# Kernel tuning notes

Hardware: AMD Instinct MI355X
Metric: run time of the kernel (lower is better)

Reference implementation:

```python
import jax, jax.numpy as jnp
import numpy as np

B, C, H, W = 1024, 3, 32, 32
NCLS = 10

def _conv(x, w, b, padding):
    y = jax.lax.conv_general_dilated(x, w, (1, 1), padding, dimension_numbers=('NCHW', 'OIHW', 'NCHW'))
    return y + b[None, :, None, None]

def _maxpool2(x):
    return jax.lax.reduce_window(x, -jnp.inf, jax.lax.max, (1, 1, 2, 2), (1, 1, 2, 2), 'VALID')

def _lenet(x, lw1, lb1, lw2, lb2, lfc1, lfb1, lfc2, lfb2, lfc3, lfb3):
    h = jax.nn.relu(_conv(x, lw1, lb1, 'VALID'))   # [B,6,28,28]
    h = _maxpool2(h)                               # [B,6,14,14]
    h = jax.nn.relu(_conv(h, lw2, lb2, 'VALID'))   # [B,16,10,10]
    h = _maxpool2(h)                               # [B,16,5,5]
    h = h.reshape(h.shape[0], -1)                  # [B,400]
    h = jax.nn.relu(h @ lfc1 + lfb1)
    h = jax.nn.relu(h @ lfc2 + lfb2)
    return h @ lfc3 + lfb3                         # [B,10]

def _resnet(x, rw0, rb0, rw1a, rb1a, rw1b, rb1b, rw2a, rb2a, rw2b, rb2b, rfc, rfb):
    h = jax.nn.relu(_conv(x, rw0, rb0, 'SAME'))    # [B,64,32,32]
    r = jax.nn.relu(_conv(h, rw1a, rb1a, 'SAME'))
    r = _conv(r, rw1b, rb1b, 'SAME')
    h = jax.nn.relu(h + r)
    r = jax.nn.relu(_conv(h, rw2a, rb2a, 'SAME'))
    r = _conv(r, rw2b, rb2b, 'SAME')
    h = jax.nn.relu(h + r)
    h = h.mean(axis=(2, 3))                        # [B,64]
    return h @ rfc + rfb                           # [B,10]

def setup_inputs():
    key = jax.random.key(0)
    ks = jax.random.split(key, 16)
    def w(k, shape, fan_in):
        return jax.random.normal(k, shape, jnp.float32) * np.float32(1.0 / np.sqrt(fan_in))
    return {
        'x': jax.random.normal(ks[0], (B, C, H, W), jnp.float32),
        'threshold': jnp.float32(0.3),
        'labels': jax.random.randint(ks[1], (B,), 0, NCLS),
        'lw1': w(ks[2], (6, 3, 5, 5), 75), 'lb1': jnp.zeros((6,), jnp.float32),
        'lw2': w(ks[3], (16, 6, 5, 5), 150), 'lb2': jnp.zeros((16,), jnp.float32),
        'lfc1': w(ks[4], (400, 120), 400), 'lfb1': jnp.zeros((120,), jnp.float32),
        'lfc2': w(ks[5], (120, 84), 120), 'lfb2': jnp.zeros((84,), jnp.float32),
        'lfc3': w(ks[6], (84, NCLS), 84), 'lfb3': jnp.zeros((NCLS,), jnp.float32),
        'rw0': w(ks[7], (64, 3, 3, 3), 27), 'rb0': jnp.zeros((64,), jnp.float32),
        'rw1a': w(ks[8], (64, 64, 3, 3), 576), 'rb1a': jnp.zeros((64,), jnp.float32),
        'rw1b': w(ks[9], (64, 64, 3, 3), 576), 'rb1b': jnp.zeros((64,), jnp.float32),
        'rw2a': w(ks[10], (64, 64, 3, 3), 576), 'rb2a': jnp.zeros((64,), jnp.float32),
        'rw2b': w(ks[11], (64, 64, 3, 3), 576), 'rb2b': jnp.zeros((64,), jnp.float32),
        'rfc': w(ks[12], (64, NCLS), 64), 'rfb': jnp.zeros((NCLS,), jnp.float32),
    }

def reference(x, threshold, labels, lw1, lb1, lw2, lb2, lfc1, lfb1, lfc2, lfb2, lfc3, lfb3, rw0, rb0, rw1a, rb1a, rw1b, rb1b, rw2a, rb2a, rw2b, rb2b, rfc, rfb):
    out = _lenet(x, lw1, lb1, lw2, lb2, lfc1, lfb1, lfc2, lfb2, lfc3, lfb3)
    pred = jnp.argmax(out, axis=1)
    # fused confusion-matrix update: single scatter-add replaces the 10x10 python loop
    conf_matrix = jnp.zeros((NCLS, NCLS), jnp.float32).at[labels, pred].add(1.0)
    probs = jax.nn.softmax(out, axis=1)
    top2, _ = jax.lax.top_k(probs, 2)
    low_conf = (top2[:, 0] - top2[:, 1]) <= threshold    # [B] bool
    # batched fallback: one grouped resnet call + masked merge replaces the per-sample loop
    res_out = _resnet(x, rw0, rb0, rw1a, rb1a, rw1b, rb1b, rw2a, rb2a, rw2b, rb2b, rfc, rfb)
    out = jnp.where(low_conf[:, None], res_out, out)
    return out, conf_matrix
```

## Files before the change

### kernel.cpp

```cpp
#include <hip/hip_runtime.h>
#include <hip/hip_bf16.h>
#include <math.h>

#define BATCH 1024

typedef __attribute__((ext_vector_type(8))) short bf16x8;
typedef __attribute__((ext_vector_type(4))) float f32x4;

#define IMG_ELEMS 73984
#define IMG_B 147968
#define ROW_B 4352
#define CH_B 544
#define WT_HALF_B 36864
#define ACT_A_OFF 73728
#define ACT_B_OFF 117248

__global__ __launch_bounds__(256) void lenet_conv1(const float* __restrict__ x,
    const float* __restrict__ w, const float* __restrict__ bias, float* __restrict__ p1)
{
    __shared__ float img[3 * 1024];
    __shared__ float wl[450];
    __shared__ float bl[6];
    int b = blockIdx.x, t = threadIdx.x;
    for (int i = t; i < 3072; i += 256) img[i] = x[(size_t)b * 3072 + i];
    for (int i = t; i < 450; i += 256) wl[i] = w[i];
    if (t < 6) bl[t] = bias[t];
    __syncthreads();
    for (int idx = t; idx < 1176; idx += 256) {
        int o = idx / 196, r = idx - o * 196, py = r / 14, px = r - py * 14;
        int y0 = 2 * py, x0 = 2 * px;
        float s00, s01, s10, s11;
        s00 = s01 = s10 = s11 = bl[o];
        for (int c = 0; c < 3; c++) {
            float pv[6][6];
            #pragma unroll
            for (int i2 = 0; i2 < 6; i2++)
                #pragma unroll
                for (int j2 = 0; j2 < 6; j2++)
                    pv[i2][j2] = img[c * 1024 + (y0 + i2) * 32 + x0 + j2];
            const float* wc = &wl[o * 75 + c * 25];
            #pragma unroll
            for (int ky = 0; ky < 5; ky++)
                #pragma unroll
                for (int kx = 0; kx < 5; kx++) {
                    float wv = wc[ky * 5 + kx];
                    s00 += pv[ky][kx] * wv;
                    s01 += pv[ky][kx + 1] * wv;
                    s10 += pv[ky + 1][kx] * wv;
                    s11 += pv[ky + 1][kx + 1] * wv;
                }
        }
        float m = fmaxf(fmaxf(s00, s01), fmaxf(s10, s11));
        p1[(size_t)b * 1176 + idx] = fmaxf(m, 0.f);
    }
}

__global__ __launch_bounds__(256) void lenet_conv2(const float* __restrict__ p1,
    const float* __restrict__ w, const float* __restrict__ bias, float* __restrict__ p2)
{
    __shared__ float img[1176];
    __shared__ float wl[2400];
    __shared__ float bl[16];
    int b = blockIdx.x, t = threadIdx.x;
    for (int i = t; i < 1176; i += 256) img[i] = p1[(size_t)b * 1176 + i];
    for (int i = t; i < 2400; i += 256) wl[i] = w[i];
    if (t < 16) bl[t] = bias[t];
    __syncthreads();
    for (int idx = t; idx < 400; idx += 256) {
        int o = idx / 25, r = idx - o * 25, py = r / 5, px = r - py * 5;
        int y0 = 2 * py, x0 = 2 * px;
        float s00, s01, s10, s11;
        s00 = s01 = s10 = s11 = bl[o];
        for (int c = 0; c < 6; c++) {
            float pv[6][6];
            #pragma unroll
            for (int i2 = 0; i2 < 6; i2++)
                #pragma unroll
                for (int j2 = 0; j2 < 6; j2++)
                    pv[i2][j2] = img[c * 196 + (y0 + i2) * 14 + x0 + j2];
            const float* wc = &wl[o * 150 + c * 25];
            #pragma unroll
            for (int ky = 0; ky < 5; ky++)
                #pragma unroll
                for (int kx = 0; kx < 5; kx++) {
                    float wv = wc[ky * 5 + kx];
                    s00 += pv[ky][kx] * wv;
                    s01 += pv[ky][kx + 1] * wv;
                    s10 += pv[ky + 1][kx] * wv;
                    s11 += pv[ky + 1][kx + 1] * wv;
                }
        }
        float m = fmaxf(fmaxf(s00, s01), fmaxf(s10, s11));
        p2[(size_t)b * 400 + idx] = fmaxf(m, 0.f);
    }
}

__global__ __launch_bounds__(256) void lenet_fc(const float* __restrict__ p2,
    const float* __restrict__ w1, const float* __restrict__ b1,
    const float* __restrict__ w2, const float* __restrict__ b2,
    const float* __restrict__ w3, const float* __restrict__ b3,
    const int* __restrict__ labels, const float* __restrict__ thr,
    float* __restrict__ out, float* __restrict__ conf, int* __restrict__ flags)
{
    __shared__ float xin[400];
    __shared__ float h1[120];
    __shared__ float h2[84];
    __shared__ float ps[256];
    __shared__ float lg[10];
    int b = blockIdx.x, t = threadIdx.x;
    for (int i = t; i < 400; i += 256) xin[i] = p2[(size_t)b * 400 + i];
    __syncthreads();
    {
        int n = t & 127, half = t >> 7;
        float s = 0.f;
        if (n < 120) {
            int k0 = half * 200;
            for (int k = k0; k < k0 + 200; k++) s += xin[k] * w1[k * 120 + n];
        }
        ps[t] = s;
    }
    __syncthreads();
    if (t < 120) h1[t] = fmaxf(ps[t] + ps[t + 128] + b1[t], 0.f);
    __syncthreads();
    {
        int n = t & 127, half = t >> 7;
        float s = 0.f;
        if (n < 84) {
            int k0 = half * 60;
            for (int k = k0; k < k0 + 60; k++) s += h1[k] * w2[k * 84 + n];
        }
        ps[t] = s;
    }
    __syncthreads();
    if (t < 84) h2[t] = fmaxf(ps[t] + ps[t + 128] + b2[t], 0.f);
    __syncthreads();
    if (t < 10) {
        float s = b3[t];
        for (int k = 0; k < 84; k++) s += h2[k] * w3[k * 10 + t];
        lg[t] = s;
        out[(size_t)b * 10 + t] = s;
    }
    __syncthreads();
    if (t == 0) {
        int pred = 0;
        float m = lg[0];
        #pragma unroll
        for (int j = 1; j < 10; j++) if (lg[j] > m) { m = lg[j]; pred = j; }
        float se = 0.f, m2 = -1e30f;
        #pragma unroll
        for (int j = 0; j < 10; j++) {
            se += expf(lg[j] - m);
            if (j != pred) m2 = fmaxf(m2, lg[j]);
        }
        float gap = (1.f - expf(m2 - m)) / se;
        flags[b] = (gap <= thr[0]) ? 1 : 0;
        atomicAdd(&conf[labels[b] * 10 + pred], 1.f);
    }
}

__global__ __launch_bounds__(256) void prep_weights(
    const float* __restrict__ w0, const float* __restrict__ w1,
    const float* __restrict__ w2, const float* __restrict__ w3,
    __hip_bfloat16* __restrict__ dst)
{
    int tid = blockIdx.x * 256 + threadIdx.x;
    if (tid >= 4 * 36864) return;
    int c = tid / 36864, r = tid - c * 36864;
    int tap = r / 4096, r2 = r - tap * 4096;
    int co = r2 >> 6, ci = r2 & 63;
    const float* src = (c == 0) ? w0 : (c == 1) ? w1 : (c == 2) ? w2 : w3;
    float v = src[((size_t)co * 64 + ci) * 9 + tap];
    int nh = co >> 5, nt = (co >> 4) & 1, m = co & 15;
    int kb = ci >> 5, q = (ci >> 3) & 3, e = ci & 7;
    size_t elem = (size_t)(c * 2 + nh) * 18432
                + (size_t)((tap * 2 + kb) * 2 + nt) * 512 + q * 128 + m * 8 + e;
    dst[elem] = __float2bfloat16(v);
}

__global__ __launch_bounds__(256) void prep_w0t(const float* __restrict__ w,
                                                float* __restrict__ dst)
{
    int tid = blockIdx.x * 256 + threadIdx.x;
    if (tid >= 1728) return;
    int k = tid >> 6, co = tid & 63;
    dst[tid] = w[co * 27 + k];
}

__global__ __launch_bounds__(256) void zero_borders(__hip_bfloat16* __restrict__ buf, int cb)
{
    int tid = blockIdx.x * 256 + threadIdx.x;
    int total = cb * 132 * 8;
    if (tid >= total) return;
    int img = tid / 1056, r = tid - img * 1056;
    int pxi = r >> 3, chunk = r & 7;
    int row, col;
    if (pxi < 34)       { row = 0;  col = pxi; }
    else if (pxi < 68)  { row = 33; col = pxi - 34; }
    else if (pxi < 100) { row = pxi - 67; col = 0; }
    else                { row = pxi - 99; col = 33; }
    uint4 z = {0, 0, 0, 0};
    *(uint4*)((char*)buf + (size_t)img * IMG_B + (size_t)row * ROW_B
              + chunk * CH_B + col * 16) = z;
}

__global__ __launch_bounds__(256) void conv0_nhwc(const float* __restrict__ x,
    const float* __restrict__ wT, const float* __restrict__ bias,
    __hip_bfloat16* __restrict__ out, int cb)
{
    __shared__ char smem[8 * ROW_B];
    float* sl = (float*)smem;
    int bid = blockIdx.x;
    int img = bid % cb, strip = bid / cb;
    int r0 = strip * 8;
    int t = threadIdx.x;
    const float* xi = x + (size_t)img * 3072;
    for (int i = t; i < 1020; i += 256) {
        int c = i / 340, rr2 = i - c * 340;
        int rr = rr2 / 34, cc = rr2 - rr * 34;
        int y = r0 + rr - 1, xx = cc - 1;
        float v = 0.f;
        if (y >= 0 && y < 32 && xx >= 0 && xx < 32) v = xi[c * 1024 + y * 32 + xx];
        sl[(c * 10 + rr) * 34 + cc] = v;
    }
    __syncthreads();

    int rr = t >> 5, col = t & 31;
    float iv[27];
    #pragma unroll
    for (int c = 0; c < 3; c++)
        #pragma unroll
        for (int dy = 0; dy < 3; dy++)
            #pragma unroll
            for (int dx = 0; dx < 3; dx++)
                iv[c * 9 + dy * 3 + dx] = sl[(c * 10 + rr + dy) * 34 + col + dx];
    __syncthreads();

    float s[64];
    #pragma unroll
    for (int co = 0; co < 64; co++) s[co] = bias[co];
    #pragma unroll
    for (int k = 0; k < 27; k++) {
        const float v = iv[k];
        const float* wk = wT + k * 64;
        #pragma unroll
        for (int co = 0; co < 64; co++) s[co] = fmaf(v, wk[co], s[co]);
    }
    __hip_bfloat16 ov[64];
    #pragma unroll
    for (int co = 0; co < 64; co++) ov[co] = __float2bfloat16(fmaxf(s[co], 0.f));

    char* brow = smem + rr * ROW_B + (col + 1) * 16;
    const uint4* srcv = (const uint4*)ov;
    #pragma unroll
    for (int j = 0; j < 8; j++) *(uint4*)(brow + j * CH_B) = srcv[j];
    if (t < 128) {
        int row = t >> 4, ch = (t >> 1) & 7, side = t & 1;
        uint4 z = {0, 0, 0, 0};
        *(uint4*)(smem + row * ROW_B + ch * CH_B + (side ? 33 : 0) * 16) = z;
    }
    __syncthreads();
    char* gbase = (char*)out + (size_t)img * IMG_B + (size_t)(r0 + 1) * ROW_B;
    for (int u = t; u < 2176; u += 256)
        *(uint4*)(gbase + (size_t)u * 16) = *(const uint4*)(smem + (size_t)u * 16);
}

#define GLL(gp, lp)                                                            \
    __builtin_amdgcn_global_load_lds(                                          \
        (const __attribute__((address_space(1))) unsigned int*)(gp),           \
        (__attribute__((address_space(3))) unsigned int*)(lp), 16, 0, 0)

template<bool ADD>
__global__ __launch_bounds__(256, 1) void conv3x3_lds(
    const __hip_bfloat16* __restrict__ act, const __hip_bfloat16* __restrict__ wts,
    const float* __restrict__ bias, const __hip_bfloat16* __restrict__ skip,
    __hip_bfloat16* __restrict__ out, int cb)
{
    __shared__ char sl[160768];
    int img = blockIdx.x;
    int t = threadIdx.x;
    int w = t >> 6, lane = t & 63;
    int m = lane & 15, q = lane >> 4;

    const char* gimg = (const char*)act + (size_t)img * IMG_B;

    const char* gw = (const char*)wts;
    for (int u0 = w * 64; u0 < 4608; u0 += 256)
        GLL(gw + (size_t)(u0 + lane) * 16, sl + u0 * 16);
    for (int u0 = w * 64; u0 < 2720; u0 += 256) {
        int u = u0 + lane;
        if (u < 2720) GLL(gimg + (size_t)u * 16, sl + ACT_A_OFF + u0 * 16);
    }
    asm volatile("s_waitcnt vmcnt(0)" ::: "memory");
    asm volatile("s_barrier" ::: "memory");

    int abase[4];
    #pragma unroll
    for (int mt = 0; mt < 4; mt++)
        abase[mt] = (2 * w + (mt >> 1)) * ROW_B + ((mt & 1) * 16 + m) * 16 + q * CH_B;
    int bbase[4];
    #pragma unroll
    for (int nt = 0; nt < 4; nt++)
        bbase[nt] = (nt >> 1) * WT_HALF_B + (nt & 1) * 1024 + q * 256 + m * 16;
    float bv[4];
    #pragma unroll
    for (int nt = 0; nt < 4; nt++) bv[nt] = bias[nt * 16 + m];

    int curo = ACT_A_OFF;
    for (int strip = 0; strip < 4; ++strip) {
        int nxto = (ACT_A_OFF + ACT_B_OFF) - curo;

        if (strip < 3) {
            const char* gn = gimg + (size_t)(strip + 1) * (8 * ROW_B);
            for (int u0 = w * 64; u0 < 2720; u0 += 256) {
                int u = u0 + lane;
                if (u < 2720) GLL(gn + (size_t)u * 16, sl + nxto + u0 * 16);
            }
        }

        f32x4 acc[4][4] = {};
        bf16x8 a[2][4], b[2][4];
        const char* ab = sl + curo;

        #define ALOAD(s, buf)                                                  \
            {                                                                  \
                const int tap_ = (s) >> 1, kb_ = (s) & 1;                      \
                const int dy_ = tap_ / 3, dx_ = tap_ - dy_ * 3;                \
                const int aoff_ = dy_ * ROW_B + kb_ * (4 * CH_B) + dx_ * 16;   \
                _Pragma("unroll")                                              \
                for (int mt = 0; mt < 4; mt++)                                 \
                    a[buf][mt] = *(const bf16x8*)(ab + abase[mt] + aoff_);     \
            }
        #define BLOAD(s, buf)                                                  \
            {                                                                  \
                const int boff_ = ((s) >> 1) * 4096 + ((s) & 1) * 2048;        \
                _Pragma("unroll")                                              \
                for (int nt = 0; nt < 4; nt++)                                 \
                    b[buf][nt] = *(const bf16x8*)(sl + bbase[nt] + boff_);     \
            }

        ALOAD(0, 0) BLOAD(0, 0)
        #pragma unroll
        for (int s = 0; s < 18; s++) {
            int cur = s & 1;
            if (s < 17) { ALOAD(s + 1, cur ^ 1) BLOAD(s + 1, cur ^ 1) }
            #pragma unroll
            for (int mt = 0; mt < 4; mt++)
                #pragma unroll
                for (int nt = 0; nt < 4; nt++)
                    acc[mt][nt] = __builtin_amdgcn_mfma_f32_16x16x32_bf16(
                        a[cur][mt], b[cur][nt], acc[mt][nt], 0, 0, 0);
        }
        #undef ALOAD
        #undef BLOAD

        asm volatile("s_waitcnt lgkmcnt(0)" ::: "memory");
        asm volatile("s_barrier" ::: "memory");

        #pragma unroll
        for (int nt = 0; nt < 4; nt++) {
            #pragma unroll
            for (int mt = 0; mt < 4; mt++) {
                int pl = (2 * w + (mt >> 1)) * 32 + (mt & 1) * 16 + q * 4;
                #pragma unroll
                for (int r = 0; r < 4; r++) {
                    __hip_bfloat16 hv = __float2bfloat16(acc[mt][nt][r] + bv[nt]);
                    *(__hip_bfloat16*)(sl + curo + (size_t)(pl + r) * 136
                                       + (nt * 16 + m) * 2) = hv;
                }
            }
        }
        asm volatile("s_waitcnt lgkmcnt(0)" ::: "memory");
        asm volatile("s_barrier" ::: "memory");

        {
            char* oimg = (char*)out + (size_t)img * IMG_B;
            const char* simg = (const char*)skip + (size_t)img * IMG_B;
            int ch = t >> 5, px = t & 31;
            #pragma unroll
            for (int pass = 0; pass < 8; pass++) {
                size_t goff = (size_t)(strip * 8 + 1 + pass) * ROW_B
                            + ch * CH_B + (px + 1) * 16;
                bf16x8 v = *(const bf16x8*)(sl + curo
                            + (size_t)(pass * 32 + px) * 136 + ch * 16);
                bf16x8 o;
                if (ADD) {
                    bf16x8 sv = *(const bf16x8*)(simg + goff);
                    #pragma unroll
                    for (int e = 0; e < 8; e++) {
                        float f = __bfloat162float(((__hip_bfloat16*)&v)[e])
                                + __bfloat162float(((__hip_bfloat16*)&sv)[e]);
                        ((__hip_bfloat16*)&o)[e] = __float2bfloat16(fmaxf(f, 0.f));
                    }
                } else {
                    #pragma unroll
                    for (int e = 0; e < 8; e++) {
                        float f = __bfloat162float(((__hip_bfloat16*)&v)[e]);
                        ((__hip_bfloat16*)&o)[e] = __float2bfloat16(fmaxf(f, 0.f));
                    }
                }
                *(bf16x8*)(oimg + goff) = o;
            }
        }

        asm volatile("s_waitcnt lgkmcnt(0)" ::: "memory");
        if (strip < 3) asm volatile("s_waitcnt vmcnt(0)" ::: "memory");
        asm volatile("s_barrier" ::: "memory");
        curo = nxto;
    }
}

__global__ __launch_bounds__(256) void res_head_bf16(const __hip_bfloat16* __restrict__ h,
    const float* __restrict__ rfc, const float* __restrict__ rfb,
    const int* __restrict__ flags, float* __restrict__ out)
{
    __shared__ float part[4][64];
    __shared__ float mns[64];
    int img = blockIdx.x, t = threadIdx.x;
    int w = t >> 6, lane = t & 63;
    int c = lane & 7;
    const char* base = (const char*)h + (size_t)img * IMG_B;

    float s8[8];
    #pragma unroll
    for (int j = 0; j < 8; j++) s8[j] = 0.f;

    for (int ry = 0; ry < 8; ry++) {
        int row = w * 8 + ry + 1;
        const char* rb = base + (size_t)row * ROW_B;
        #pragma unroll
        for (int k = 0; k < 4; k++) {
            int g = lane + 64 * k;
            bf16x8 v = *(const bf16x8*)(rb + c * CH_B + ((g >> 3) + 1) * 16);
            #pragma unroll
            for (int j = 0; j < 8; j++)
                s8[j] += __bfloat162float(*(__hip_bfloat16*)&((short*)&v)[j]);
        }
    }
    #pragma unroll
    for (int off = 8; off <= 32; off <<= 1)
        #pragma unroll
        for (int j = 0; j < 8; j++) s8[j] += __shfl_xor(s8[j], off, 64);
    if (lane < 8)
        #pragma unroll
        for (int j = 0; j < 8; j++) part[w][c * 8 + j] = s8[j];
    __syncthreads();
    if (t < 64) mns[t] = (part[0][t] + part[1][t] + part[2][t] + part[3][t]) * (1.f / 1024.f);
    __syncthreads();
    if (t < 10 && flags[img]) {
        float s2 = rfb[t];
        for (int cc = 0; cc < 64; cc++) s2 += mns[cc] * rfc[cc * 10 + t];
        out[(size_t)img * 10 + t] = s2;
    }
}

extern "C" void kernel_launch(void* const* d_in, const int* in_sizes, int n_in,
                              void* d_out, int out_size, void* d_ws, size_t ws_size,
                              hipStream_t stream)
{
    const float* x    = (const float*)d_in[0];
    const float* thr  = (const float*)d_in[1];
    const int*   labels = (const int*)d_in[2];
    const float* lw1 = (const float*)d_in[3];  const float* lb1 = (const float*)d_in[4];
    const float* lw2 = (const float*)d_in[5];  const float* lb2 = (const float*)d_in[6];
    const float* lfc1 = (const float*)d_in[7]; const float* lfb1 = (const float*)d_in[8];
    const float* lfc2 = (const float*)d_in[9]; const float* lfb2 = (const float*)d_in[10];
    const float* lfc3 = (const float*)d_in[11];const float* lfb3 = (const float*)d_in[12];
    const float* rw0 = (const float*)d_in[13]; const float* rb0 = (const float*)d_in[14];
    const float* rw1a = (const float*)d_in[15];const float* rb1a = (const float*)d_in[16];
    const float* rw1b = (const float*)d_in[17];const float* rb1b = (const float*)d_in[18];
    const float* rw2a = (const float*)d_in[19];const float* rb2a = (const float*)d_in[20];
    const float* rw2b = (const float*)d_in[21];const float* rb2b = (const float*)d_in[22];
    const float* rfc = (const float*)d_in[23]; const float* rfb = (const float*)d_in[24];

    float* out  = (float*)d_out;
    float* conf = out + (size_t)BATCH * 10;

    int nc = 1;
    while (nc < 16 &&
           2ull * (size_t)(BATCH / nc) * 147968ull + 294912ull + 16384ull > ws_size)
        nc <<= 1;
    int cb = BATCH / nc;

    __hip_bfloat16* A  = (__hip_bfloat16*)d_ws;
    __hip_bfloat16* Bb = A + (size_t)cb * IMG_ELEMS;
    __hip_bfloat16* wprep = Bb + (size_t)cb * IMG_ELEMS;
    int* flags = (int*)((char*)wprep + 294912);
    float* w0t = (float*)((char*)wprep + 294912 + 4096);

    float* p1 = (float*)A;
    float* p2 = p1 + 1204224;

    hipMemsetAsync(conf, 0, 100 * sizeof(float), stream);

    prep_weights<<<(4 * 36864 + 255) / 256, 256, 0, stream>>>(rw1a, rw1b, rw2a, rw2b, wprep);
    prep_w0t<<<7, 256, 0, stream>>>(rw0, w0t);

    lenet_conv1<<<BATCH, 256, 0, stream>>>(x, lw1, lb1, p1);
    lenet_conv2<<<BATCH, 256, 0, stream>>>(p1, lw2, lb2, p2);
    lenet_fc<<<BATCH, 256, 0, stream>>>(p2, lfc1, lfb1, lfc2, lfb2, lfc3, lfb3,
                                        labels, thr, out, conf, flags);

    int zb = (cb * 1056 + 255) / 256;
    zero_borders<<<zb, 256, 0, stream>>>(A, cb);
    zero_borders<<<zb, 256, 0, stream>>>(Bb, cb);

    const __hip_bfloat16* W1a = wprep;
    const __hip_bfloat16* W1b = wprep + 36864;
    const __hip_bfloat16* W2a = wprep + 2 * 36864;
    const __hip_bfloat16* W2b = wprep + 3 * 36864;

    for (int c0 = 0; c0 < BATCH; c0 += cb) {
        const float* xc = x + (size_t)c0 * 3072;
        conv0_nhwc<<<cb * 4, 256, 0, stream>>>(xc, w0t, rb0, A, cb);
        conv3x3_lds<false><<<cb, 256, 0, stream>>>(A,  W1a, rb1a, nullptr, Bb, cb);
        conv3x3_lds<true ><<<cb, 256, 0, stream>>>(Bb, W1b, rb1b, A, A, cb);
        conv3x3_lds<false><<<cb, 256, 0, stream>>>(A,  W2a, rb2a, nullptr, Bb, cb);
        conv3x3_lds<true ><<<cb, 256, 0, stream>>>(Bb, W2b, rb2b, A, A, cb);
        res_head_bf16<<<cb, 256, 0, stream>>>(A, rfc, rfb, flags + c0, out + (size_t)c0 * 10);
    }
}
```

Before: 730.1 us.

## Swap MFMA operands so the conv epilogue writes straight to global memory

```diff
diff --git a/kernel.cpp b/kernel.cpp
--- a/kernel.cpp
+++ b/kernel.cpp
@@ -293,17 +293,21 @@
     asm volatile("s_waitcnt vmcnt(0)" ::: "memory");
     asm volatile("s_barrier" ::: "memory");
 
-    int abase[4];
+    int xbase[4];
+    #pragma unroll
+    for (int nt = 0; nt < 4; nt++)
+        xbase[nt] = (2 * w + (nt >> 1)) * ROW_B + ((nt & 1) * 16 + m) * 16 + q * CH_B;
+    int wbase[4];
     #pragma unroll
     for (int mt = 0; mt < 4; mt++)
-        abase[mt] = (2 * w + (mt >> 1)) * ROW_B + ((mt & 1) * 16 + m) * 16 + q * CH_B;
-    int bbase[4];
-    #pragma unroll
-    for (int nt = 0; nt < 4; nt++)
-        bbase[nt] = (nt >> 1) * WT_HALF_B + (nt & 1) * 1024 + q * 256 + m * 16;
-    float bv[4];
-    #pragma unroll
-    for (int nt = 0; nt < 4; nt++) bv[nt] = bias[nt * 16 + m];
+        wbase[mt] = (mt >> 1) * WT_HALF_B + (mt & 1) * 1024 + q * 256 + m * 16;
+    float4 bv4[4];
+    #pragma unroll
+    for (int mt = 0; mt < 4; mt++)
+        bv4[mt] = *(const float4*)(bias + (mt >> 1) * 32 + (mt & 1) * 16 + q * 4);
+
+    char* oimg = (char*)out + (size_t)img * IMG_B;
+    const char* simg = (const char*)skip + (size_t)img * IMG_B;
 
     int curo = ACT_A_OFF;
     for (int strip = 0; strip < 4; ++strip) {
@@ -321,90 +325,71 @@
         bf16x8 a[2][4], b[2][4];
         const char* ab = sl + curo;
 
-        #define ALOAD(s, buf)                                                  \
+        #define XLOAD(s, buf)                                                  \
             {                                                                  \
                 const int tap_ = (s) >> 1, kb_ = (s) & 1;                      \
-                const int dy_ = tap_ / 3, dx_ = tap_ - dy_ * 3;                \
-                const int aoff_ = dy_ * ROW_B + kb_ * (4 * CH_B) + dx_ * 16;   \
+                const int off_ = (tap_ / 3) * ROW_B                            \
+                               + (tap_ - (tap_ / 3) * 3) * 16                  \
+                               + kb_ * (4 * CH_B);                             \
+                _Pragma("unroll")                                              \
+                for (int nt = 0; nt < 4; nt++)                                 \
+                    a[buf][nt] = *(const bf16x8*)(ab + xbase[nt] + off_);      \
+            }
+        #define WLOAD(s, buf)                                                  \
+            {                                                                  \
+                const int off_ = ((s) >> 1) * 4096 + ((s) & 1) * 2048;         \
                 _Pragma("unroll")                                              \
                 for (int mt = 0; mt < 4; mt++)                                 \
-                    a[buf][mt] = *(const bf16x8*)(ab + abase[mt] + aoff_);     \
+                    b[buf][mt] = *(const bf16x8*)(sl + wbase[mt] + off_);      \
             }
-        #define BLOAD(s, buf)                                                  \
-            {                                                                  \
-                const int boff_ = ((s) >> 1) * 4096 + ((s) & 1) * 2048;        \
-                _Pragma("unroll")                                              \
-                for (int nt = 0; nt < 4; nt++)                                 \
-                    b[buf][nt] = *(const bf16x8*)(sl + bbase[nt] + boff_);     \
-            }
-
-        ALOAD(0, 0) BLOAD(0, 0)
+
+        XLOAD(0, 0) WLOAD(0, 0)
         #pragma unroll
         for (int s = 0; s < 18; s++) {
             int cur = s & 1;
-            if (s < 17) { ALOAD(s + 1, cur ^ 1) BLOAD(s + 1, cur ^ 1) }
+            if (s < 17) { XLOAD(s + 1, cur ^ 1) WLOAD(s + 1, cur ^ 1) }
             #pragma unroll
             for (int mt = 0; mt < 4; mt++)
                 #pragma unroll
                 for (int nt = 0; nt < 4; nt++)
                     acc[mt][nt] = __builtin_amdgcn_mfma_f32_16x16x32_bf16(
-                        a[cur][mt], b[cur][nt], acc[mt][nt], 0, 0, 0);
-        }
-        #undef ALOAD
-        #undef BLOAD
-
-        asm volatile("s_waitcnt lgkmcnt(0)" ::: "memory");
-        asm volatile("s_barrier" ::: "memory");
-
-        #pragma unroll
-        for (int nt = 0; nt < 4; nt++) {
-            #pragma unroll
-            for (int mt = 0; mt < 4; mt++) {
-                int pl = (2 * w + (mt >> 1)) * 32 + (mt & 1) * 16 + q * 4;
-                #pragma unroll
-                for (int r = 0; r < 4; r++) {
-                    __hip_bfloat16 hv = __float2bfloat16(acc[mt][nt][r] + bv[nt]);
-                    *(__hip_bfloat16*)(sl + curo + (size_t)(pl + r) * 136
-                                       + (nt * 16 + m) * 2) = hv;
-                }
-            }
-        }
-        asm volatile("s_waitcnt lgkmcnt(0)" ::: "memory");
-        asm volatile("s_barrier" ::: "memory");
-
-        {
-            char* oimg = (char*)out + (size_t)img * IMG_B;
-            const char* simg = (const char*)skip + (size_t)img * IMG_B;
-            int ch = t >> 5, px = t & 31;
-            #pragma unroll
-            for (int pass = 0; pass < 8; pass++) {
-                size_t goff = (size_t)(strip * 8 + 1 + pass) * ROW_B
-                            + ch * CH_B + (px + 1) * 16;
-                bf16x8 v = *(const bf16x8*)(sl + curo
-                            + (size_t)(pass * 32 + px) * 136 + ch * 16);
-                bf16x8 o;
+                        b[cur][mt], a[cur][nt], acc[mt][nt], 0, 0, 0);
+        }
+        #undef XLOAD
+        #undef WLOAD
+
+        #pragma unroll
+        for (int mt = 0; mt < 4; mt++) {
+            #pragma unroll
+            for (int nt = 0; nt < 4; nt++) {
+                size_t goff = (size_t)(strip * 8 + 1 + 2 * w + (nt >> 1)) * ROW_B
+                            + ((mt >> 1) * 4 + (mt & 1) * 2 + (q >> 1)) * CH_B
+                            + (m + (nt & 1) * 16 + 1) * 16 + (q & 1) * 8;
+                union { uint2 u; __hip_bfloat16 h[4]; } pk;
                 if (ADD) {
-                    bf16x8 sv = *(const bf16x8*)(simg + goff);
+                    union { uint2 u; __hip_bfloat16 h[4]; } sk;
+                    sk.u = *(const uint2*)(simg + goff);
                     #pragma unroll
-                    for (int e = 0; e < 8; e++) {
-                        float f = __bfloat162float(((__hip_bfloat16*)&v)[e])
-                                + __bfloat162float(((__hip_bfloat16*)&sv)[e]);
-                        ((__hip_bfloat16*)&o)[e] = __float2bfloat16(fmaxf(f, 0.f));
+                    for (int r = 0; r < 4; r++) {
+                        float f = acc[mt][nt][r] + ((const float*)&bv4[mt])[r]
+                                + __bfloat162float(sk.h[r]);
+                        pk.h[r] = __float2bfloat16(fmaxf(f, 0.f));
                     }
                 } else {
                     #pragma unroll
-                    for (int e = 0; e < 8; e++) {
-                        float f = __bfloat162float(((__hip_bfloat16*)&v)[e]);
-                        ((__hip_bfloat16*)&o)[e] = __float2bfloat16(fmaxf(f, 0.f));
+                    for (int r = 0; r < 4; r++) {
+                        float f = acc[mt][nt][r] + ((const float*)&bv4[mt])[r];
+                        pk.h[r] = __float2bfloat16(fmaxf(f, 0.f));
                     }
                 }
-                *(bf16x8*)(oimg + goff) = o;
+                *(uint2*)(oimg + goff) = pk.u;
             }
         }
 
-        asm volatile("s_waitcnt lgkmcnt(0)" ::: "memory");
-        if (strip < 3) asm volatile("s_waitcnt vmcnt(0)" ::: "memory");
-        asm volatile("s_barrier" ::: "memory");
+        if (strip < 3) {
+            asm volatile("s_waitcnt vmcnt(0)" ::: "memory");
+            asm volatile("s_barrier" ::: "memory");
+        }
         curo = nxto;
     }
 }
```

New measurement: 790.3 us. +8.2%, slower.
